# Performance work log

Measured on AMD Instinct MI355X. Metric: run time of the kernel, lower is better.

## Reference

```python
import jax, jax.numpy as jnp
import numpy as np

TEMPERATURE = 0.5
NEG_FILL = -9e15


def setup_inputs() -> dict:
    key = jax.random.key(0)
    k1, k2 = jax.random.split(key)
    B, D = 8192, 128
    z_i = jax.random.normal(k1, (B, D), dtype=jnp.float32)
    z_j = jax.random.normal(k2, (B, D), dtype=jnp.float32)
    return {"z_i": z_i, "z_j": z_j}


def reference(z_i, z_j):
    B = z_i.shape[0]
    N = 2 * B
    z = jnp.concatenate([z_i, z_j], axis=0)              # [2B, D]
    sim = jnp.matmul(z, z.T) / TEMPERATURE               # [2B, 2B]
    # mask out self-similarity on the diagonal
    diag = jnp.eye(N, dtype=bool)
    sim = jnp.where(diag, NEG_FILL, sim)
    # positive pair of row k is row (k+B) mod 2B
    labels = jnp.concatenate([jnp.arange(B, N), jnp.arange(0, B)])
    # CrossEntropyLoss(reduction='sum'): sum_k logsumexp(sim[k]) - sim[k, labels[k]]
    lse = jax.nn.logsumexp(sim, axis=1)                  # [2B]
    pos = sim[jnp.arange(N), labels]                     # [2B]
    loss = jnp.sum(lse - pos)
    return loss / N
```

## Files before the change

kernel.cpp:

```cpp
#include <hip/hip_runtime.h>

#define TEMP    0.5f
#define LOG2E   1.4426950408889634f
#define C2      (LOG2E / TEMP)
#define MSHIFT  160.0f
#define LN2     0.6931471805599453f
#define NROWS   16384
#define BHALF   8192
#define DDIM    128
#define PREPB   2048

typedef __bf16 bf16x8 __attribute__((ext_vector_type(8)));
typedef float  f32x16 __attribute__((ext_vector_type(16)));
typedef float  f32x2  __attribute__((ext_vector_type(2)));

__device__ __forceinline__ float fexp2(float x) {
#if __has_builtin(__builtin_amdgcn_exp2f)
  return __builtin_amdgcn_exp2f(x);
#else
  return exp2f(x);
#endif
}

__device__ __forceinline__ unsigned short f2bf(float f) {
  unsigned int u = __float_as_uint(f);
  unsigned int r = (u + 0x7FFFu + ((u >> 16) & 1u)) >> 16;
  return (unsigned short)r;
}


__global__ void k_prep(const float* __restrict__ zi, const float* __restrict__ zj,
                       unsigned short* __restrict__ zbF,
                       float* __restrict__ S, float* __restrict__ Pp) {
  const int t   = blockIdx.x * 256 + threadIdx.x;
  const int row = t >> 5;
  const int k0  = (t & 31) * 4;
  const float* src = (row < BHALF) ? (zi + (size_t)row * DDIM)
                                   : (zj + (size_t)(row - BHALF) * DDIM);
  float4 v = *reinterpret_cast<const float4*>(src + k0);

  const int g = row >> 5, lo = row & 31, khi = k0 >> 3, j0 = k0 & 7;
  ushort4 o;
  o.x = f2bf(v.x); o.y = f2bf(v.y); o.z = f2bf(v.z); o.w = f2bf(v.w);
  *reinterpret_cast<ushort4*>(zbF + (size_t)g * 4096 + khi * 256 + lo * 8 + j0) = o;

  float dot = 0.f;
  if (row < BHALF) {
    float4 w = *reinterpret_cast<const float4*>(zj + (size_t)row * DDIM + k0);
    dot = fmaf(v.x, w.x, fmaf(v.y, w.y, fmaf(v.z, w.z, v.w * w.w)));
  }
#pragma unroll
  for (int m = 32; m >= 1; m >>= 1) dot += __shfl_xor(dot, m, 64);
  __shared__ float red[4];
  if ((threadIdx.x & 63) == 0) red[threadIdx.x >> 6] = dot;
  __syncthreads();
  if (threadIdx.x == 0) Pp[blockIdx.x] = red[0] + red[1] + red[2] + red[3];

  if (t < NROWS) S[t] = 0.f;
}

template <bool MASK>
__device__ __forceinline__ void expAcc(const f32x16& acc, f32x2& s, int d, int hi) {
#pragma unroll
  for (int k = 0; k < 8; ++k) {
    f32x2 u;
    u.x = acc[2 * k];
    u.y = acc[2 * k + 1];
    const f32x2 c2v = {C2, C2};
    const f32x2 msv = {-MSHIFT, -MSHIFT};
    u = __builtin_elementwise_fma(u, c2v, msv);
    f32x2 e;
    e.x = fexp2(u.x);
    e.y = fexp2(u.y);
    if (MASK) {
      const int r0 = 2 * k, r1 = 2 * k + 1;
      if (((r0 & 3) + 8 * (r0 >> 2) + 4 * hi) == d) e.x = 0.f;
      if (((r1 & 3) + 8 * (r1 >> 2) + 4 * hi) == d) e.y = 0.f;
    }
    s += e;
  }
}

#define MFMA_ __builtin_amdgcn_mfma_f32_32x32x16_bf16

__global__ __launch_bounds__(256, 2)
void k_main(const unsigned short* __restrict__ zbF, float* __restrict__ S) {
  const int wave = threadIdx.x >> 6;
  const int lane = threadIdx.x & 63;
  const int lo = lane & 31;
  const int hi = lane >> 5;
  const int rb = blockIdx.x & 31;
  const int cc = blockIdx.x >> 5;
  const int row0w = rb * 512 + wave * 128;

  bf16x8 b[4][8];
#pragma unroll
  for (int rt = 0; rt < 4; ++rt) {
    const unsigned short* bp = zbF + (size_t)((row0w >> 5) + rt) * 4096 + hi * 256 + lo * 8;
#pragma unroll
    for (int ks = 0; ks < 8; ++ks)
      b[rt][ks] = *reinterpret_cast<const bf16x8*>(bp + ks * 512);
  }

  const f32x16 kZ = {};
  f32x2 s[4];
#pragma unroll
  for (int rt = 0; rt < 4; ++rt) { s[rt].x = 0.f; s[rt].y = 0.f; }

  const int c0base = cc * 1024;
  const unsigned short* abase = zbF + (size_t)(c0base >> 5) * 4096 + hi * 256 + lo * 8;

  bf16x8 a[8];
#pragma unroll
  for (int ks = 0; ks < 8; ++ks)
    a[ks] = *reinterpret_cast<const bf16x8*>(abase + ks * 512);

  if (((blockIdx.x >> 8) & 1) != 0) __builtin_amdgcn_s_sleep(7);

  for (int it = 0; it < 32; ++it) {
    const int c0 = c0base + it * 32;
    const int dr = c0 - row0w;
    const bool dg = (unsigned)dr < 128u;
    const int rtd = dg ? (dr >> 5) : -1;

    __builtin_amdgcn_s_setprio(1);
    f32x16 acc0 = MFMA_(a[0], b[0][0], kZ, 0, 0, 0);
    f32x16 acc1 = MFMA_(a[0], b[1][0], kZ, 0, 0, 0);
#pragma unroll
    for (int ks = 1; ks < 8; ++ks) {
      acc0 = MFMA_(a[ks], b[0][ks], acc0, 0, 0, 0);
      acc1 = MFMA_(a[ks], b[1][ks], acc1, 0, 0, 0);
    }
    __builtin_amdgcn_s_setprio(0);
    if (!dg) {
      expAcc<false>(acc0, s[0], -1, hi);
      expAcc<false>(acc1, s[1], -1, hi);
    } else {
      expAcc<true>(acc0, s[0], rtd == 0 ? lo : -1, hi);
      expAcc<true>(acc1, s[1], rtd == 1 ? lo : -1, hi);
    }

    __builtin_amdgcn_s_setprio(1);
    acc0 = MFMA_(a[0], b[2][0], kZ, 0, 0, 0);
    acc1 = MFMA_(a[0], b[3][0], kZ, 0, 0, 0);
#pragma unroll
    for (int ks = 1; ks < 8; ++ks) {
      acc0 = MFMA_(a[ks], b[2][ks], acc0, 0, 0, 0);
      acc1 = MFMA_(a[ks], b[3][ks], acc1, 0, 0, 0);
    }
    __builtin_amdgcn_s_setprio(0);

    if (it + 1 < 32) {
      const unsigned short* ap = abase + (size_t)(it + 1) * 4096;
#pragma unroll
      for (int ks = 0; ks < 8; ++ks)
        a[ks] = *reinterpret_cast<const bf16x8*>(ap + ks * 512);
    }

    if (!dg) {
      expAcc<false>(acc0, s[2], -1, hi);
      expAcc<false>(acc1, s[3], -1, hi);
    } else {
      expAcc<true>(acc0, s[2], rtd == 2 ? lo : -1, hi);
      expAcc<true>(acc1, s[3], rtd == 3 ? lo : -1, hi);
    }
  }

#pragma unroll
  for (int rt = 0; rt < 4; ++rt) {
    float v = s[rt].x + s[rt].y;
    v += __shfl_xor(v, 32, 64);
    if (hi == 0) atomicAdd(&S[row0w + rt * 32 + lo], v);
  }
}

__global__ void k_fin(const float* __restrict__ S, const float* __restrict__ Pp,
                      float* __restrict__ out) {
  const int t = threadIdx.x;
  float q = 0.f;
  for (int r = t; r < NROWS; r += 1024)
    q += LN2 * (MSHIFT + __log2f(S[r]));
  for (int r = t; r < PREPB; r += 1024)
    q -= 4.0f * Pp[r];
  __shared__ float red[1024];
  red[t] = q;
  __syncthreads();
  for (int s2 = 512; s2 > 0; s2 >>= 1) {
    if (t < s2) red[t] += red[t + s2];
    __syncthreads();
  }
  if (t == 0) out[0] = red[0] / (float)NROWS;
}

extern "C" void kernel_launch(void* const* d_in, const int* in_sizes, int n_in,
                              void* d_out, int out_size, void* d_ws, size_t ws_size,
                              hipStream_t stream) {
  const float* zi = (const float*)d_in[0];
  const float* zj = (const float*)d_in[1];
  unsigned short* zbF = (unsigned short*)d_ws;
  float* S  = (float*)((char*)d_ws + (size_t)NROWS * DDIM * 2);
  float* Pp = S + NROWS;
  float* out = (float*)d_out;

  hipLaunchKernelGGL(k_prep, dim3(PREPB), dim3(256), 0, stream, zi, zj, zbF, S, Pp);
  hipLaunchKernelGGL(k_main, dim3(512),  dim3(256), 0, stream, zbF, S);
  hipLaunchKernelGGL(k_fin,  dim3(1),    dim3(1024), 0, stream, S, Pp, out);
}
```

Before: 132.4 us.

## Software-pipeline MFMA and exp across double-buffered accumulators, halve grid

```diff
diff --git a/kernel.cpp b/kernel.cpp
--- a/kernel.cpp
+++ b/kernel.cpp
@@ -59,31 +59,116 @@
   if (t < NROWS) S[t] = 0.f;
 }
 
+
 template <bool MASK>
-__device__ __forceinline__ void expAcc(const f32x16& acc, f32x2& s, int d, int hi) {
+__device__ __forceinline__ void expStep(const f32x16& e, int k, f32x2& s,
+                                        int d, int hi) {
+  f32x2 u;
+  u.x = e[2 * k];
+  u.y = e[2 * k + 1];
+  const f32x2 c2v = {C2, C2};
+  const f32x2 msv = {-MSHIFT, -MSHIFT};
+  u = __builtin_elementwise_fma(u, c2v, msv);
+  f32x2 ev;
+  ev.x = fexp2(u.x);
+  ev.y = fexp2(u.y);
+  if (MASK) {
+    const int r0 = 2 * k, r1 = 2 * k + 1;
+    if (((r0 & 3) + 8 * (r0 >> 2) + 4 * hi) == d) ev.x = 0.f;
+    if (((r1 & 3) + 8 * (r1 >> 2) + 4 * hi) == d) ev.y = 0.f;
+  }
+  s += ev;
+}
+
+#define MFMA_ __builtin_amdgcn_mfma_f32_32x32x16_bf16
+
+template <bool MASK, bool RELOAD>
+__device__ __forceinline__ void phase(const bf16x8 (&aC)[8], bf16x8 (&aN)[8],
+                                      const bf16x8 (&b)[4][8], const f32x16& kZ,
+                                      f32x16& x0, f32x16& x1, f32x16& x2, f32x16& x3,
+                                      const f32x16& e0, const f32x16& e1,
+                                      const f32x16& e2, const f32x16& e3,
+                                      f32x2 (&s)[4],
+                                      const unsigned short* __restrict__ rp,
+                                      int d0, int d1, int d2, int d3, int hi) {
+  x0 = MFMA_(aC[0], b[0][0], kZ, 0, 0, 0);
+  x1 = MFMA_(aC[0], b[1][0], kZ, 0, 0, 0);
+  x2 = MFMA_(aC[0], b[2][0], kZ, 0, 0, 0);
+  x3 = MFMA_(aC[0], b[3][0], kZ, 0, 0, 0);
+  if constexpr (RELOAD) aN[0] = *reinterpret_cast<const bf16x8*>(rp);
+  expStep<MASK>(e0, 0, s[0], d0, hi);
+  expStep<MASK>(e1, 0, s[1], d1, hi);
+  expStep<MASK>(e2, 0, s[2], d2, hi);
+  expStep<MASK>(e3, 0, s[3], d3, hi);
+#pragma unroll
+  for (int ks = 1; ks < 8; ++ks) {
+    x0 = MFMA_(aC[ks], b[0][ks], x0, 0, 0, 0);
+    x1 = MFMA_(aC[ks], b[1][ks], x1, 0, 0, 0);
+    x2 = MFMA_(aC[ks], b[2][ks], x2, 0, 0, 0);
+    x3 = MFMA_(aC[ks], b[3][ks], x3, 0, 0, 0);
+    if constexpr (RELOAD)
+      aN[ks] = *reinterpret_cast<const bf16x8*>(rp + (size_t)ks * 512);
+    expStep<MASK>(e0, ks, s[0], d0, hi);
+    expStep<MASK>(e1, ks, s[1], d1, hi);
+    expStep<MASK>(e2, ks, s[2], d2, hi);
+    expStep<MASK>(e3, ks, s[3], d3, hi);
+  }
+}
+
+template <bool RELOAD>
+__device__ __forceinline__ void phaseD(const bf16x8 (&aC)[8], bf16x8 (&aN)[8],
+                                       const bf16x8 (&b)[4][8], const f32x16& kZ,
+                                       f32x16& x0, f32x16& x1, f32x16& x2, f32x16& x3,
+                                       const f32x16& e0, const f32x16& e1,
+                                       const f32x16& e2, const f32x16& e3,
+                                       f32x2 (&s)[4],
+                                       const unsigned short* __restrict__ rp,
+                                       int drE, int lo, int hi) {
+  if ((unsigned)drE >= 128u) {
+    phase<false, RELOAD>(aC, aN, b, kZ, x0, x1, x2, x3, e0, e1, e2, e3, s, rp,
+                         -1, -1, -1, -1, hi);
+  } else {
+    const int rtd = drE >> 5;
+    phase<true, RELOAD>(aC, aN, b, kZ, x0, x1, x2, x3, e0, e1, e2, e3, s, rp,
+                        rtd == 0 ? lo : -1, rtd == 1 ? lo : -1,
+                        rtd == 2 ? lo : -1, rtd == 3 ? lo : -1, hi);
+  }
+}
+
+__device__ __forceinline__ void buildPre(const bf16x8 (&aC)[8], bf16x8 (&aN)[8],
+                                         const bf16x8 (&b)[4][8], const f32x16& kZ,
+                                         f32x16& x0, f32x16& x1, f32x16& x2, f32x16& x3,
+                                         const unsigned short* __restrict__ rp) {
+  x0 = MFMA_(aC[0], b[0][0], kZ, 0, 0, 0);
+  x1 = MFMA_(aC[0], b[1][0], kZ, 0, 0, 0);
+  x2 = MFMA_(aC[0], b[2][0], kZ, 0, 0, 0);
+  x3 = MFMA_(aC[0], b[3][0], kZ, 0, 0, 0);
+  aN[0] = *reinterpret_cast<const bf16x8*>(rp);
+#pragma unroll
+  for (int ks = 1; ks < 8; ++ks) {
+    x0 = MFMA_(aC[ks], b[0][ks], x0, 0, 0, 0);
+    x1 = MFMA_(aC[ks], b[1][ks], x1, 0, 0, 0);
+    x2 = MFMA_(aC[ks], b[2][ks], x2, 0, 0, 0);
+    x3 = MFMA_(aC[ks], b[3][ks], x3, 0, 0, 0);
+    aN[ks] = *reinterpret_cast<const bf16x8*>(rp + (size_t)ks * 512);
+  }
+}
+
+template <bool MASK>
+__device__ __forceinline__ void expAll(const f32x16& e0, const f32x16& e1,
+                                       const f32x16& e2, const f32x16& e3,
+                                       f32x2 (&s)[4], int d0, int d1, int d2,
+                                       int d3, int hi) {
 #pragma unroll
   for (int k = 0; k < 8; ++k) {
-    f32x2 u;
-    u.x = acc[2 * k];
-    u.y = acc[2 * k + 1];
-    const f32x2 c2v = {C2, C2};
-    const f32x2 msv = {-MSHIFT, -MSHIFT};
-    u = __builtin_elementwise_fma(u, c2v, msv);
-    f32x2 e;
-    e.x = fexp2(u.x);
-    e.y = fexp2(u.y);
-    if (MASK) {
-      const int r0 = 2 * k, r1 = 2 * k + 1;
-      if (((r0 & 3) + 8 * (r0 >> 2) + 4 * hi) == d) e.x = 0.f;
-      if (((r1 & 3) + 8 * (r1 >> 2) + 4 * hi) == d) e.y = 0.f;
-    }
-    s += e;
-  }
-}
-
-#define MFMA_ __builtin_amdgcn_mfma_f32_32x32x16_bf16
-
-__global__ __launch_bounds__(256, 2)
+    expStep<MASK>(e0, k, s[0], d0, hi);
+    expStep<MASK>(e1, k, s[1], d1, hi);
+    expStep<MASK>(e2, k, s[2], d2, hi);
+    expStep<MASK>(e3, k, s[3], d3, hi);
+  }
+}
+
+__global__ __launch_bounds__(256, 1)
 void k_main(const unsigned short* __restrict__ zbF, float* __restrict__ S) {
   const int wave = threadIdx.x >> 6;
   const int lane = threadIdx.x & 63;
@@ -107,62 +192,36 @@
 #pragma unroll
   for (int rt = 0; rt < 4; ++rt) { s[rt].x = 0.f; s[rt].y = 0.f; }
 
-  const int c0base = cc * 1024;
+  const int c0base = cc * 2048;
   const unsigned short* abase = zbF + (size_t)(c0base >> 5) * 4096 + hi * 256 + lo * 8;
 
-  bf16x8 a[8];
+  bf16x8 aA[8], aB[8];
 #pragma unroll
   for (int ks = 0; ks < 8; ++ks)
-    a[ks] = *reinterpret_cast<const bf16x8*>(abase + ks * 512);
-
-  if (((blockIdx.x >> 8) & 1) != 0) __builtin_amdgcn_s_sleep(7);
-
-  for (int it = 0; it < 32; ++it) {
-    const int c0 = c0base + it * 32;
-    const int dr = c0 - row0w;
-    const bool dg = (unsigned)dr < 128u;
-    const int rtd = dg ? (dr >> 5) : -1;
-
-    __builtin_amdgcn_s_setprio(1);
-    f32x16 acc0 = MFMA_(a[0], b[0][0], kZ, 0, 0, 0);
-    f32x16 acc1 = MFMA_(a[0], b[1][0], kZ, 0, 0, 0);
-#pragma unroll
-    for (int ks = 1; ks < 8; ++ks) {
-      acc0 = MFMA_(a[ks], b[0][ks], acc0, 0, 0, 0);
-      acc1 = MFMA_(a[ks], b[1][ks], acc1, 0, 0, 0);
-    }
-    __builtin_amdgcn_s_setprio(0);
-    if (!dg) {
-      expAcc<false>(acc0, s[0], -1, hi);
-      expAcc<false>(acc1, s[1], -1, hi);
+    aA[ks] = *reinterpret_cast<const bf16x8*>(abase + ks * 512);
+
+  f32x16 xA0, xA1, xA2, xA3, xB0, xB1, xB2, xB3;
+
+  buildPre(aA, aB, b, kZ, xA0, xA1, xA2, xA3, abase + (size_t)4096);
+
+  for (int p = 0; p < 31; ++p) {
+    const int it1 = 2 * p + 1;
+    const int it2 = 2 * p + 2;
+    phaseD<true>(aB, aA, b, kZ, xB0, xB1, xB2, xB3, xA0, xA1, xA2, xA3, s,
+                 abase + (size_t)it2 * 4096, c0base + 2 * p * 32 - row0w, lo, hi);
+    phaseD<true>(aA, aB, b, kZ, xA0, xA1, xA2, xA3, xB0, xB1, xB2, xB3, s,
+                 abase + (size_t)(it2 + 1) * 4096, c0base + it1 * 32 - row0w, lo, hi);
+  }
+  phaseD<false>(aB, aA, b, kZ, xB0, xB1, xB2, xB3, xA0, xA1, xA2, xA3, s,
+                abase, c0base + 62 * 32 - row0w, lo, hi);
+  {
+    const int drE = c0base + 63 * 32 - row0w;
+    if ((unsigned)drE >= 128u) {
+      expAll<false>(xB0, xB1, xB2, xB3, s, -1, -1, -1, -1, hi);
     } else {
-      expAcc<true>(acc0, s[0], rtd == 0 ? lo : -1, hi);
-      expAcc<true>(acc1, s[1], rtd == 1 ? lo : -1, hi);
-    }
-
-    __builtin_amdgcn_s_setprio(1);
-    acc0 = MFMA_(a[0], b[2][0], kZ, 0, 0, 0);
-    acc1 = MFMA_(a[0], b[3][0], kZ, 0, 0, 0);
-#pragma unroll
-    for (int ks = 1; ks < 8; ++ks) {
-      acc0 = MFMA_(a[ks], b[2][ks], acc0, 0, 0, 0);
-      acc1 = MFMA_(a[ks], b[3][ks], acc1, 0, 0, 0);
-    }
-    __builtin_amdgcn_s_setprio(0);
-
-    if (it + 1 < 32) {
-      const unsigned short* ap = abase + (size_t)(it + 1) * 4096;
-#pragma unroll
-      for (int ks = 0; ks < 8; ++ks)
-        a[ks] = *reinterpret_cast<const bf16x8*>(ap + ks * 512);
-    }
-
-    if (!dg) {
-      expAcc<false>(acc0, s[2], -1, hi);
-      expAcc<false>(acc1, s[3], -1, hi);
-    } else {
-      expAcc<true>(acc0, s[2], rtd == 2 ? lo : -1, hi);
-      expAcc<true>(acc1, s[3], rtd == 3 ? lo : -1, hi);
+      const int rtd = drE >> 5;
+      expAll<true>(xB0, xB1, xB2, xB3, s, rtd == 0 ? lo : -1, rtd == 1 ? lo : -1,
+                   rtd == 2 ? lo : -1, rtd == 3 ? lo : -1, hi);
     }
   }
 
@@ -203,6 +262,6 @@
   float* out = (float*)d_out;
 
   hipLaunchKernelGGL(k_prep, dim3(PREPB), dim3(256), 0, stream, zi, zj, zbF, S, Pp);
-  hipLaunchKernelGGL(k_main, dim3(512),  dim3(256), 0, stream, zbF, S);
+  hipLaunchKernelGGL(k_main, dim3(256),  dim3(256), 0, stream, zbF, S);
   hipLaunchKernelGGL(k_fin,  dim3(1),    dim3(1024), 0, stream, S, Pp, out);
 }
```

Result: slower. 135.9 us (+2.6%).
